# Performance work log

Measured on AMD Instinct MI355X. Metric: run time of the kernel, lower is better.

Reference implementation:

```python
import jax, jax.numpy as jnp
import numpy as np

H = 16           # num_heads
D = 1024         # num_units
QD = KD = VD = 64
LN_EPS = 1e-5


def _xavier(key, shape):
    fan_in, fan_out = shape[-2], shape[-1]
    std = np.sqrt(2.0 / (fan_in + fan_out))
    return jax.random.normal(key, shape, dtype=jnp.float32) * std


def setup_inputs() -> dict:
    key = jax.random.key(0)
    ks = jax.random.split(key, 10)
    B, Sq, Sk = 8, 1024, 1024
    return {
        "query": jax.random.normal(ks[0], (B, Sq, D), dtype=jnp.float32),
        "keys": jax.random.normal(ks[1], (B, Sk, D), dtype=jnp.float32),
        "values": jax.random.normal(ks[2], (B, Sk, D), dtype=jnp.float32),
        "Wq": _xavier(ks[3], (H, D, QD)),
        "Wk": _xavier(ks[4], (H, D, KD)),
        "Wv": _xavier(ks[5], (H, D, VD)),
        "Wp": _xavier(ks[6], (H * VD, D)),   # proj, stored input-major: y = x @ Wp + bp
        "bp": jnp.zeros((D,), dtype=jnp.float32),
        "gamma": jnp.ones((D,), dtype=jnp.float32),
        "beta": jnp.zeros((D,), dtype=jnp.float32),
    }


def reference(query, keys, values, Wq, Wk, Wv, Wp, bp, gamma, beta):
    B, Sq, _ = query.shape
    Sk = keys.shape[1]
    # RepeatLinear per head: [B,S,D] x [H,D,e] -> [H,B,S,e]
    Q = jnp.einsum("bsd,hde->hbse", query, Wq)
    K = jnp.einsum("bsd,hde->hbse", keys, Wk)
    V = jnp.einsum("bsd,hde->hbse", values, Wv)
    # NOTE: original scales by sqrt(num_units), not sqrt(key_dim)
    temper = jnp.asarray(np.sqrt(D), dtype=Q.dtype)
    scores = jnp.einsum("hbqe,hbke->hbqk", Q, K) / temper  # [H,B,Sq,Sk]
    attn = jax.nn.softmax(scores, axis=-1)
    # dropout is identity in eval mode
    out = jnp.einsum("hbqk,hbke->hbqe", attn, V)           # [H,B,Sq,VD]
    # torch.cat(torch.split(out, B, 0), -1): head-major feature concat
    out = out.transpose(1, 2, 0, 3).reshape(B, Sq, H * VD)
    out = out @ Wp + bp                                     # proj
    # residual + LayerNorm
    y = out + query
    mu = jnp.mean(y, axis=-1, keepdims=True)
    var = jnp.var(y, axis=-1, keepdims=True)
    y = (y - mu) / jnp.sqrt(var + LN_EPS) * gamma + beta
    return y, attn.reshape(H * B, Sq, Sk)
```

## Files before the change

### kernel.cpp

```cpp
#include <hip/hip_runtime.h>
#include <hip/hip_bf16.h>

#define H_ 16
#define B_ 8
#define S_ 1024
#define D_ 1024
#define E_ 64
#define HB_ 128
#define LN_EPS 1e-5f
#define LOG2E 1.4426950408889634f

typedef unsigned short u16;
typedef __bf16 bf16x8 __attribute__((ext_vector_type(8)));
typedef u16 u16x8 __attribute__((ext_vector_type(8)));
typedef u16 u16x4 __attribute__((ext_vector_type(4)));
typedef float f32x4 __attribute__((ext_vector_type(4)));

#define MFMA16(a, b, c) __builtin_amdgcn_mfma_f32_16x16x32_bf16( \
    __builtin_bit_cast(bf16x8, (a)), __builtin_bit_cast(bf16x8, (b)), (c), 0, 0, 0)

#define GLL16(gp, lp) __builtin_amdgcn_global_load_lds( \
    (const __attribute__((address_space(1))) void*)(gp), \
    (__attribute__((address_space(3))) void*)(lp), 16, 0, 0)

__device__ __forceinline__ u16 f2bf(float x) {
  union { float f; unsigned u; } v; v.f = x;
  unsigned r = v.u + 0x7fffu + ((v.u >> 16) & 1u);
  return (u16)(r >> 16);
}

__device__ __forceinline__ unsigned cvt_pk_bf16(float lo, float hi) {
  unsigned r;
  asm("v_cvt_pk_bf16_f32 %0, %1, %2" : "=v"(r) : "v"(lo), "v"(hi));
  return r;
}
__device__ __forceinline__ u16x4 pk4(f32x4 v) {
  union { unsigned u[2]; u16x4 s; } r;
  r.u[0] = cvt_pk_bf16(v[0], v[1]);
  r.u[1] = cvt_pk_bf16(v[2], v[3]);
  return r.s;
}
__device__ __forceinline__ float exp2_hw(float x) {
  float r;
  asm("v_exp_f32 %0, %1" : "=v"(r) : "v"(x));
  return r;
}

__global__ __launch_bounds__(256) void k_transpose_all(
    const float* __restrict__ Wq, const float* __restrict__ Wk,
    const float* __restrict__ Wv, const float* __restrict__ Wp,
    u16* __restrict__ Wt) {
  __shared__ float tile[64][65];
  const int bid = blockIdx.x;
  const int which = bid >> 8, r = bid & 255;
  const float* src;
  int R, C, rt, ct;
  float scale = 1.0f;
  size_t soff, doff;
  if (which < 3) {
    src = which == 0 ? Wq : which == 1 ? Wk : Wv;
    if (which == 0) scale = LOG2E / 32.0f;
    int slice = r & 15, rtile = r >> 4;
    R = 1024; C = 64; rt = rtile * 64; ct = 0;
    soff = (size_t)slice * 65536;
    doff = (size_t)which * (1 << 20) + (size_t)slice * 65536;
  } else {
    src = Wp;
    R = 1024; C = 1024; rt = (r & 15) * 64; ct = (r >> 4) * 64;
    soff = 0; doff = (size_t)3 * (1 << 20);
  }
  const float* I = src + soff;
  u16* O = Wt + doff;
  const int t = threadIdx.x;
  const int c4 = (t & 15) * 4;
  #pragma unroll
  for (int i = 0; i < 4; i++) {
    int rr = i * 16 + (t >> 4);
    f32x4 v = *(const f32x4*)&I[(size_t)(rt + rr) * C + ct + c4];
    tile[rr][c4 + 0] = v[0]; tile[rr][c4 + 1] = v[1];
    tile[rr][c4 + 2] = v[2]; tile[rr][c4 + 3] = v[3];
  }
  __syncthreads();
  #pragma unroll
  for (int i = 0; i < 4; i++) {
    int oc = i * 16 + (t >> 4);
    f32x4 tv;
    #pragma unroll
    for (int rr = 0; rr < 4; rr++) tv[rr] = tile[c4 + rr][oc] * scale;
    *(u16x4*)&O[(size_t)(ct + oc) * R + rt + c4] = pk4(tv);
  }
}

__global__ void k_convert3(const float* __restrict__ Xq, const float* __restrict__ Xk,
    const float* __restrict__ Xv, u16* __restrict__ dst) {
  const int bid = blockIdx.x;
  const int t = bid >> 12;
  const float* X = t == 0 ? Xq : t == 1 ? Xk : Xv;
  u16* Y = dst + (size_t)t * (8 << 20);
  int i = ((bid & 4095) * 256 + threadIdx.x) * 8;
  f32x4 a = *(const f32x4*)(X + i);
  f32x4 b = *(const f32x4*)(X + i + 4);
  union { unsigned u[4]; u16x8 s; } v;
  v.u[0] = cvt_pk_bf16(a[0], a[1]);
  v.u[1] = cvt_pk_bf16(a[2], a[3]);
  v.u[2] = cvt_pk_bf16(b[0], b[1]);
  v.u[3] = cvt_pk_bf16(b[2], b[3]);
  *(u16x8*)(Y + i) = v.s;
}

#define STAGE_TILES() do { \
    GLL16(Ag + kt,             AsB0); \
    GLL16(Ag + 64 * 1024 + kt, AsB0 + 2048); \
    GLL16(Bg + kt,             BsB0); \
    GLL16(Bg + 64 * 1024 + kt, BsB0 + 2048); \
  } while (0)

#define READ_FRAGS() do { \
    _Pragma("unroll") \
    for (int mi = 0; mi < 4; mi++) \
      af[mi] = *(const u16x8*)&As[(wr * 64 + mi * 16 + lr) * 32 + lg * 8]; \
    _Pragma("unroll") \
    for (int ni = 0; ni < 4; ni++) \
      bf[ni] = *(const u16x8*)&Bs[(wc * 64 + ni * 16 + lr) * 32 + lg * 8]; \
  } while (0)

template<int MODE>
__global__ __launch_bounds__(256) void k_gemm(
    const u16* __restrict__ X0, const u16* __restrict__ Ball,
    u16* __restrict__ O0, u16* __restrict__ O1, u16* __restrict__ O2,
    float* __restrict__ Pf, const float* __restrict__ bp,
    const float* __restrict__ query) {
  const int bid = blockIdx.x + (blockIdx.y << 6);
  const int bx  = ((bid & 7) << 3) + ((bid >> 3) & 7);
  const int by  = bid >> 6;
  const int l  = threadIdx.x & 63;
  const int w  = threadIdx.x >> 6;
  const int lr = l & 15, lg = l >> 4;
  const int wr = w >> 1, wc = w & 1;
  const int m0 = bx * 128, n0 = by * 128;

  const u16* A = (MODE == 0) ? X0 + (size_t)(by >> 3) * (8 << 20) : X0;

  __shared__ __align__(16) u16 As[128 * 32];
  __shared__ __align__(16) u16 Bs[128 * 32];

  const int srow = w * 16 + (l >> 2);
  const int scol = (l & 3) * 8;
  const u16* Ag = A    + (size_t)(m0 + srow) * 1024 + scol;
  const u16* Bg = Ball + (size_t)(n0 + srow) * 1024 + scol;
  u16* AsB0 = As + w * 512;
  u16* BsB0 = Bs + w * 512;

  f32x4 acc[4][4] = {};
  u16x8 af[4], bf[4];

  if (MODE == 2 || by < 16) {
    for (int kt = 0; kt < 1024; kt += 32) {
      STAGE_TILES();
      __syncthreads();
      READ_FRAGS();
      #pragma unroll
      for (int mi = 0; mi < 4; mi++)
        #pragma unroll
        for (int ni = 0; ni < 4; ni++)
          acc[mi][ni] = MFMA16(bf[ni], af[mi], acc[mi][ni]);
      __syncthreads();
    }
  } else {
    for (int kt = 0; kt < 1024; kt += 32) {
      STAGE_TILES();
      __syncthreads();
      READ_FRAGS();
      #pragma unroll
      for (int mi = 0; mi < 4; mi++)
        #pragma unroll
        for (int ni = 0; ni < 4; ni++)
          acc[mi][ni] = MFMA16(af[mi], bf[ni], acc[mi][ni]);
      __syncthreads();
    }
  }

  if (MODE == 0 && by < 16) {
    u16* Out = (by >= 8) ? O1 : O0;
    const int h = (by & 7) * 2 + wc;
    #pragma unroll
    for (int mi = 0; mi < 4; mi++) {
      int s = m0 + wr * 64 + mi * 16 + lr;
      int bb = s >> 10, ss = s & 1023;
      #pragma unroll
      for (int ni = 0; ni < 4; ni++)
        *(u16x4*)&Out[((size_t)(h * 8 + bb) * 1024 + ss) * 64 + ni * 16 + lg * 4] =
            pk4(acc[mi][ni]);
    }
  } else if (MODE == 0) {
    const int byv = by - 16;
    const int h = byv * 2 + wc;
    #pragma unroll
    for (int mi = 0; mi < 4; mi++) {
      int s = m0 + wr * 64 + mi * 16 + lg * 4;
      int bb = s >> 10, ss = s & 1023;
      #pragma unroll
      for (int ni = 0; ni < 4; ni++)
        *(u16x4*)&O2[((size_t)(h * 8 + bb) * 64 + ni * 16 + lr) * 1024 + ss] =
            pk4(acc[mi][ni]);
    }
  } else {
    #pragma unroll
    for (int mi = 0; mi < 4; mi++) {
      int m = m0 + wr * 64 + mi * 16 + lr;
      #pragma unroll
      for (int ni = 0; ni < 4; ni++) {
        int n = n0 + wc * 64 + ni * 16 + lg * 4;
        f32x4 b4 = *(const f32x4*)(bp + n);
        f32x4 q4 = *(const f32x4*)(query + (size_t)m * 1024 + n);
        f32x4 o = acc[mi][ni] + b4 + q4;
        *(f32x4*)(Pf + (size_t)m * 1024 + n) = o;
      }
    }
  }
}

__global__ __launch_bounds__(256, 4) void k_attn(const u16* __restrict__ Qb,
    const u16* __restrict__ Kb, const u16* __restrict__ Vtb,
    float* __restrict__ attn_out, u16* __restrict__ AO) {
  const int bid = blockIdx.x;
  const int xcd = bid & 7, within = bid >> 3;
  const int qt = within & 63;
  const int hb = xcd * 16 + (within >> 6);
  const int w  = threadIdx.x >> 6;
  const int l  = threadIdx.x & 63;
  const int lr = l & 15, lg = l >> 4;
  const int q0 = qt * 16;

  __shared__ __align__(16) u16 pbuf[16 * 1024];
  __shared__ float wmaxs[4][16];
  __shared__ float wsums[4][16];

  const u16* Qp = Qb + ((size_t)hb * 1024 + q0 + lr) * 64 + lg * 8;
  const u16* Kp = Kb + ((size_t)hb * 1024 + w * 256 + lr) * 64 + lg * 8;
  u16x8 q_lo = *(const u16x8*)Qp;
  u16x8 q_hi = *(const u16x8*)(Qp + 32);

  f32x4 sacc[16] = {};
  __builtin_amdgcn_s_setprio(1);
  #pragma unroll
  for (int j = 0; j < 16; j++) {
    u16x8 k0 = *(const u16x8*)(Kp + (size_t)j * 16 * 64);
    u16x8 k1 = *(const u16x8*)(Kp + (size_t)j * 16 * 64 + 32);
    sacc[j] = MFMA16(k0, q_lo, sacc[j]);
    sacc[j] = MFMA16(k1, q_hi, sacc[j]);
  }
  __builtin_amdgcn_s_setprio(0);

  float mx = sacc[0][0];
  #pragma unroll
  for (int j = 0; j < 16; j++)
    #pragma unroll
    for (int r = 0; r < 4; r++) mx = fmaxf(mx, sacc[j][r]);
  mx = fmaxf(mx, __shfl_xor(mx, 16));
  mx = fmaxf(mx, __shfl_xor(mx, 32));

  float sum = 0.f;
  #pragma unroll
  for (int j = 0; j < 16; j++)
    #pragma unroll
    for (int r = 0; r < 4; r++) {
      float p = exp2_hw(sacc[j][r] - mx);
      sacc[j][r] = p;
      sum += p;
    }
  sum += __shfl_xor(sum, 16);
  sum += __shfl_xor(sum, 32);

  const u16* Vp = Vtb + ((size_t)hb * 64 + w * 16 + lr) * 1024 + lg * 8;
  u16x8 vp0 = *(const u16x8*)(Vp + 0);
  u16x8 vp1 = *(const u16x8*)(Vp + 32);
  u16x8 vp2 = *(const u16x8*)(Vp + 64);
  u16x8 vp3 = *(const u16x8*)(Vp + 96);

  #pragma unroll
  for (int j = 0; j < 16; j++) {
    int k0 = w * 256 + j * 16 + lg * 4;
    int byte = (lr * 2048 + k0 * 2) ^ ((lr & 7) << 4);
    *(u16x4*)((char*)pbuf + byte) = pk4(sacc[j]);
  }
  if (l < 16) { wmaxs[w][lr] = mx; wsums[w][lr] = sum; }

  __syncthreads();

  float m0v = wmaxs[0][lr], m1v = wmaxs[1][lr], m2v = wmaxs[2][lr], m3v = wmaxs[3][lr];
  float gmax = fmaxf(fmaxf(m0v, m1v), fmaxf(m2v, m3v));
  float e0 = exp2_hw(m0v - gmax), e1 = exp2_hw(m1v - gmax);
  float e2 = exp2_hw(m2v - gmax), e3 = exp2_hw(m3v - gmax);
  float gsum = wsums[0][lr] * e0 + wsums[1][lr] * e1 + wsums[2][lr] * e2 + wsums[3][lr] * e3;
  float inv = 1.0f / gsum;
  float c0 = e0 * inv, c1 = e1 * inv, c2 = e2 * inv, c3 = e3 * inv;
  float scale_own = exp2_hw(mx - gmax) * inv;

  float* Ap = attn_out + ((size_t)hb * 1024 + q0 + lr) * 1024 + w * 256 + lg * 4;
  #pragma unroll
  for (int j = 0; j < 16; j++) {
    f32x4 v = sacc[j] * scale_own;
    __builtin_nontemporal_store(v, (f32x4*)(Ap + j * 16));
  }

  f32x4 o0 = {}, o1 = {}, o2 = {}, o3 = {};
  __builtin_amdgcn_s_setprio(1);
  #pragma unroll
  for (int i = 0; i < 4; i++)
    #pragma unroll
    for (int kk = 0; kk < 8; kk++) {
      int kb = i * 256 + kk * 32 + lg * 8;
      int byte = (lr * 2048 + kb * 2) ^ ((lr & 7) << 4);
      u16x8 p = *(u16x8*)((char*)pbuf + byte);
      u16x8 v;
      if (i == 0 && kk == 0) v = vp0;
      else if (i == 0 && kk == 1) v = vp1;
      else if (i == 0 && kk == 2) v = vp2;
      else if (i == 0 && kk == 3) v = vp3;
      else v = *(const u16x8*)(Vp + i * 256 + kk * 32);
      if (i == 0) o0 = MFMA16(v, p, o0);
      else if (i == 1) o1 = MFMA16(v, p, o1);
      else if (i == 2) o2 = MFMA16(v, p, o2);
      else o3 = MFMA16(v, p, o3);
    }
  __builtin_amdgcn_s_setprio(0);

  const int bb = hb & 7, hh = hb >> 3;
  f32x4 oc;
  #pragma unroll
  for (int r = 0; r < 4; r++)
    oc[r] = o0[r] * c0 + o1[r] * c1 + o2[r] * c2 + o3[r] * c3;
  *(u16x4*)&AO[((size_t)bb * 1024 + q0 + lr) * 1024 + hh * 64 + w * 16 + lg * 4] = pk4(oc);
}

__global__ __launch_bounds__(256) void k_ln(const float* __restrict__ P,
    const float* __restrict__ gamma, const float* __restrict__ beta,
    float* __restrict__ y) {
  const int row = blockIdx.x * 4 + (threadIdx.x >> 6);
  const int l = threadIdx.x & 63;
  const float* p = P + (size_t)row * 1024 + l * 4;
  f32x4 v[4];
  float s = 0.f, s2 = 0.f;
  #pragma unroll
  for (int i = 0; i < 4; i++) {
    v[i] = *(const f32x4*)(p + i * 256);
    #pragma unroll
    for (int r = 0; r < 4; r++) { s += v[i][r]; s2 += v[i][r] * v[i][r]; }
  }
  #pragma unroll
  for (int off = 1; off < 64; off <<= 1) {
    s += __shfl_xor(s, off);
    s2 += __shfl_xor(s2, off);
  }
  float mu = s * (1.0f / 1024.0f);
  float var = s2 * (1.0f / 1024.0f) - mu * mu;
  float rstd = rsqrtf(var + LN_EPS);
  float* yp = y + (size_t)row * 1024 + l * 4;
  #pragma unroll
  for (int i = 0; i < 4; i++) {
    f32x4 g = *(const f32x4*)(gamma + l * 4 + i * 256);
    f32x4 b = *(const f32x4*)(beta + l * 4 + i * 256);
    f32x4 o;
    #pragma unroll
    for (int r = 0; r < 4; r++) o[r] = (v[i][r] - mu) * rstd * g[r] + b[r];
    __builtin_nontemporal_store(o, (f32x4*)(yp + i * 256));
  }
}

extern "C" void kernel_launch(void* const* d_in, const int* in_sizes, int n_in,
                              void* d_out, int out_size, void* d_ws, size_t ws_size,
                              hipStream_t stream) {
  const float* query  = (const float*)d_in[0];
  const float* keys   = (const float*)d_in[1];
  const float* values = (const float*)d_in[2];
  const float* Wq     = (const float*)d_in[3];
  const float* Wk     = (const float*)d_in[4];
  const float* Wv     = (const float*)d_in[5];
  const float* Wp     = (const float*)d_in[6];
  const float* bp     = (const float*)d_in[7];
  const float* gamma  = (const float*)d_in[8];
  const float* beta   = (const float*)d_in[9];

  float* y        = (float*)d_out;
  float* attn_out = (float*)d_out + (size_t)B_ * S_ * D_;

  u16* ws  = (u16*)d_ws;
  u16* Wqt = ws;
  u16* Wpt = Wqt + (3 << 20);
  u16* Xqb = Wqt + (4 << 20);
  u16* Qb  = Xqb + (24 << 20);
  u16* Kb  = Qb + (8 << 20);
  u16* Vtb = Kb + (8 << 20);
  u16* AO  = Vtb + (8 << 20);
  float* P = (float*)Xqb;

  k_transpose_all<<<1024, 256, 0, stream>>>(Wq, Wk, Wv, Wp, Wqt);
  k_convert3<<<12288, 256, 0, stream>>>(query, keys, values, Xqb);

  k_gemm<0><<<dim3(64, 24), 256, 0, stream>>>(Xqb, Wqt, Qb, Kb, Vtb, nullptr, nullptr, nullptr);

  k_attn<<<8192, 256, 0, stream>>>(Qb, Kb, Vtb, attn_out, AO);

  k_gemm<2><<<dim3(64, 8), 256, 0, stream>>>(AO, Wpt, nullptr, nullptr, nullptr, P, bp, query);
  k_ln<<<2048, 256, 0, stream>>>(P, gamma, beta, y);
}
```

Measured before the change: 413.6 us.

## Merge prep kernels, deepen GEMM K-tile to 64, defer attn-prob stores

Fuses the weight-transpose and input-convert kernels into one launch, removing a kernel boundary. The GEMM now stages a 64-wide K slice per iteration, halving the barrier count and doubling LDS per block, which may reduce occupancy. In attention, the V prefetch is dropped and the large fp32 probability stores are moved after the PV MFMA loop so they no longer compete with it.

Result: slower. 455.8 us (+10.2%).

```diff
diff --git a/kernel.cpp b/kernel.cpp
--- a/kernel.cpp
+++ b/kernel.cpp
@@ -23,12 +23,6 @@
     (const __attribute__((address_space(1))) void*)(gp), \
     (__attribute__((address_space(3))) void*)(lp), 16, 0, 0)
 
-__device__ __forceinline__ u16 f2bf(float x) {
-  union { float f; unsigned u; } v; v.f = x;
-  unsigned r = v.u + 0x7fffu + ((v.u >> 16) & 1u);
-  return (u16)(r >> 16);
-}
-
 __device__ __forceinline__ unsigned cvt_pk_bf16(float lo, float hi) {
   unsigned r;
   asm("v_cvt_pk_bf16_f32 %0, %1, %2" : "=v"(r) : "v"(lo), "v"(hi));
@@ -46,12 +40,30 @@
   return r;
 }
 
-__global__ __launch_bounds__(256) void k_transpose_all(
+__global__ __launch_bounds__(256) void k_prep(
     const float* __restrict__ Wq, const float* __restrict__ Wk,
     const float* __restrict__ Wv, const float* __restrict__ Wp,
-    u16* __restrict__ Wt) {
+    u16* __restrict__ Wt,
+    const float* __restrict__ Xq, const float* __restrict__ Xk,
+    const float* __restrict__ Xv, u16* __restrict__ Xdst) {
+  const int bid = blockIdx.x;
+  if (bid >= 1024) {
+    const int b2 = bid - 1024;
+    const int t = b2 >> 12;
+    const float* X = t == 0 ? Xq : t == 1 ? Xk : Xv;
+    u16* Y = Xdst + (size_t)t * (8 << 20);
+    int i = ((b2 & 4095) * 256 + threadIdx.x) * 8;
+    f32x4 a = *(const f32x4*)(X + i);
+    f32x4 b = *(const f32x4*)(X + i + 4);
+    union { unsigned u[4]; u16x8 s; } v;
+    v.u[0] = cvt_pk_bf16(a[0], a[1]);
+    v.u[1] = cvt_pk_bf16(a[2], a[3]);
+    v.u[2] = cvt_pk_bf16(b[0], b[1]);
+    v.u[3] = cvt_pk_bf16(b[2], b[3]);
+    *(u16x8*)(Y + i) = v.s;
+    return;
+  }
   __shared__ float tile[64][65];
-  const int bid = blockIdx.x;
   const int which = bid >> 8, r = bid & 255;
   const float* src;
   int R, C, rt, ct;
@@ -91,37 +103,21 @@
   }
 }
 
-__global__ void k_convert3(const float* __restrict__ Xq, const float* __restrict__ Xk,
-    const float* __restrict__ Xv, u16* __restrict__ dst) {
-  const int bid = blockIdx.x;
-  const int t = bid >> 12;
-  const float* X = t == 0 ? Xq : t == 1 ? Xk : Xv;
-  u16* Y = dst + (size_t)t * (8 << 20);
-  int i = ((bid & 4095) * 256 + threadIdx.x) * 8;
-  f32x4 a = *(const f32x4*)(X + i);
-  f32x4 b = *(const f32x4*)(X + i + 4);
-  union { unsigned u[4]; u16x8 s; } v;
-  v.u[0] = cvt_pk_bf16(a[0], a[1]);
-  v.u[1] = cvt_pk_bf16(a[2], a[3]);
-  v.u[2] = cvt_pk_bf16(b[0], b[1]);
-  v.u[3] = cvt_pk_bf16(b[2], b[3]);
-  *(u16x8*)(Y + i) = v.s;
-}
-
-#define STAGE_TILES() do { \
-    GLL16(Ag + kt,             AsB0); \
-    GLL16(Ag + 64 * 1024 + kt, AsB0 + 2048); \
-    GLL16(Bg + kt,             BsB0); \
-    GLL16(Bg + 64 * 1024 + kt, BsB0 + 2048); \
+#define STAGE64() do { \
+    _Pragma("unroll") \
+    for (int i = 0; i < 4; i++) { \
+      GLL16(Ag + (size_t)i * 8 * 1024 + kt, AsB0 + i * 512); \
+      GLL16(Bg + (size_t)i * 8 * 1024 + kt, BsB0 + i * 512); \
+    } \
   } while (0)
 
-#define READ_FRAGS() do { \
+#define READ_FRAGS64(kk) do { \
     _Pragma("unroll") \
     for (int mi = 0; mi < 4; mi++) \
-      af[mi] = *(const u16x8*)&As[(wr * 64 + mi * 16 + lr) * 32 + lg * 8]; \
+      af[mi] = *(const u16x8*)&As[(wr * 64 + mi * 16 + lr) * 64 + (kk) * 32 + lg * 8]; \
     _Pragma("unroll") \
     for (int ni = 0; ni < 4; ni++) \
-      bf[ni] = *(const u16x8*)&Bs[(wc * 64 + ni * 16 + lr) * 32 + lg * 8]; \
+      bf[ni] = *(const u16x8*)&Bs[(wc * 64 + ni * 16 + lr) * 64 + (kk) * 32 + lg * 8]; \
   } while (0)
 
 template<int MODE>
@@ -141,41 +137,47 @@
 
   const u16* A = (MODE == 0) ? X0 + (size_t)(by >> 3) * (8 << 20) : X0;
 
-  __shared__ __align__(16) u16 As[128 * 32];
-  __shared__ __align__(16) u16 Bs[128 * 32];
-
-  const int srow = w * 16 + (l >> 2);
-  const int scol = (l & 3) * 8;
-  const u16* Ag = A    + (size_t)(m0 + srow) * 1024 + scol;
-  const u16* Bg = Ball + (size_t)(n0 + srow) * 1024 + scol;
-  u16* AsB0 = As + w * 512;
-  u16* BsB0 = Bs + w * 512;
+  __shared__ __align__(16) u16 As[128 * 64];
+  __shared__ __align__(16) u16 Bs[128 * 64];
+
+  const int srow = l >> 3;
+  const int scol = (l & 7) * 8;
+  const u16* Ag = A    + (size_t)(m0 + w * 32 + srow) * 1024 + scol;
+  const u16* Bg = Ball + (size_t)(n0 + w * 32 + srow) * 1024 + scol;
+  u16* AsB0 = As + w * 2048;
+  u16* BsB0 = Bs + w * 2048;
 
   f32x4 acc[4][4] = {};
   u16x8 af[4], bf[4];
 
   if (MODE == 2 || by < 16) {
-    for (int kt = 0; kt < 1024; kt += 32) {
-      STAGE_TILES();
+    for (int kt = 0; kt < 1024; kt += 64) {
+      STAGE64();
       __syncthreads();
-      READ_FRAGS();
-      #pragma unroll
-      for (int mi = 0; mi < 4; mi++)
+      #pragma unroll
+      for (int kk = 0; kk < 2; kk++) {
+        READ_FRAGS64(kk);
         #pragma unroll
-        for (int ni = 0; ni < 4; ni++)
-          acc[mi][ni] = MFMA16(bf[ni], af[mi], acc[mi][ni]);
+        for (int mi = 0; mi < 4; mi++)
+          #pragma unroll
+          for (int ni = 0; ni < 4; ni++)
+            acc[mi][ni] = MFMA16(bf[ni], af[mi], acc[mi][ni]);
+      }
       __syncthreads();
     }
   } else {
-    for (int kt = 0; kt < 1024; kt += 32) {
-      STAGE_TILES();
+    for (int kt = 0; kt < 1024; kt += 64) {
+      STAGE64();
       __syncthreads();
-      READ_FRAGS();
-      #pragma unroll
-      for (int mi = 0; mi < 4; mi++)
+      #pragma unroll
+      for (int kk = 0; kk < 2; kk++) {
+        READ_FRAGS64(kk);
         #pragma unroll
-        for (int ni = 0; ni < 4; ni++)
-          acc[mi][ni] = MFMA16(af[mi], bf[ni], acc[mi][ni]);
+        for (int mi = 0; mi < 4; mi++)
+          #pragma unroll
+          for (int ni = 0; ni < 4; ni++)
+            acc[mi][ni] = MFMA16(af[mi], bf[ni], acc[mi][ni]);
+      }
       __syncthreads();
     }
   }
@@ -272,12 +274,6 @@
   sum += __shfl_xor(sum, 16);
   sum += __shfl_xor(sum, 32);
 
-  const u16* Vp = Vtb + ((size_t)hb * 64 + w * 16 + lr) * 1024 + lg * 8;
-  u16x8 vp0 = *(const u16x8*)(Vp + 0);
-  u16x8 vp1 = *(const u16x8*)(Vp + 32);
-  u16x8 vp2 = *(const u16x8*)(Vp + 64);
-  u16x8 vp3 = *(const u16x8*)(Vp + 96);
-
   #pragma unroll
   for (int j = 0; j < 16; j++) {
     int k0 = w * 256 + j * 16 + lg * 4;
@@ -297,13 +293,7 @@
   float c0 = e0 * inv, c1 = e1 * inv, c2 = e2 * inv, c3 = e3 * inv;
   float scale_own = exp2_hw(mx - gmax) * inv;
 
-  float* Ap = attn_out + ((size_t)hb * 1024 + q0 + lr) * 1024 + w * 256 + lg * 4;
-  #pragma unroll
-  for (int j = 0; j < 16; j++) {
-    f32x4 v = sacc[j] * scale_own;
-    __builtin_nontemporal_store(v, (f32x4*)(Ap + j * 16));
-  }
-
+  const u16* Vp = Vtb + ((size_t)hb * 64 + w * 16 + lr) * 1024 + lg * 8;
   f32x4 o0 = {}, o1 = {}, o2 = {}, o3 = {};
   __builtin_amdgcn_s_setprio(1);
   #pragma unroll
@@ -313,12 +303,7 @@
       int kb = i * 256 + kk * 32 + lg * 8;
       int byte = (lr * 2048 + kb * 2) ^ ((lr & 7) << 4);
       u16x8 p = *(u16x8*)((char*)pbuf + byte);
-      u16x8 v;
-      if (i == 0 && kk == 0) v = vp0;
-      else if (i == 0 && kk == 1) v = vp1;
-      else if (i == 0 && kk == 2) v = vp2;
-      else if (i == 0 && kk == 3) v = vp3;
-      else v = *(const u16x8*)(Vp + i * 256 + kk * 32);
+      u16x8 v = *(const u16x8*)(Vp + i * 256 + kk * 32);
       if (i == 0) o0 = MFMA16(v, p, o0);
       else if (i == 1) o1 = MFMA16(v, p, o1);
       else if (i == 2) o2 = MFMA16(v, p, o2);
@@ -332,6 +317,13 @@
   for (int r = 0; r < 4; r++)
     oc[r] = o0[r] * c0 + o1[r] * c1 + o2[r] * c2 + o3[r] * c3;
   *(u16x4*)&AO[((size_t)bb * 1024 + q0 + lr) * 1024 + hh * 64 + w * 16 + lg * 4] = pk4(oc);
+
+  float* Ap = attn_out + ((size_t)hb * 1024 + q0 + lr) * 1024 + w * 256 + lg * 4;
+  #pragma unroll
+  for (int j = 0; j < 16; j++) {
+    f32x4 v = sacc[j] * scale_own;
+    __builtin_nontemporal_store(v, (f32x4*)(Ap + j * 16));
+  }
 }
 
 __global__ __launch_bounds__(256) void k_ln(const float* __restrict__ P,
@@ -395,8 +387,7 @@
   u16* AO  = Vtb + (8 << 20);
   float* P = (float*)Xqb;
 
-  k_transpose_all<<<1024, 256, 0, stream>>>(Wq, Wk, Wv, Wp, Wqt);
-  k_convert3<<<12288, 256, 0, stream>>>(query, keys, values, Xqb);
+  k_prep<<<13312, 256, 0, stream>>>(Wq, Wk, Wv, Wp, Wqt, query, keys, values, Xqb);
 
   k_gemm<0><<<dim3(64, 24), 256, 0, stream>>>(Xqb, Wqt, Qb, Kb, Vtb, nullptr, nullptr, nullptr);
 
```
